# Kernel optimization log

Hardware: AMD Instinct MI355X
Metric: run time of the kernel (lower is better)

## Reference

```python
import jax, jax.numpy as jnp
import numpy as np

TOP_K = 2


def setup_inputs() -> dict:
    key = jax.random.key(0)
    ks = jax.random.split(key, 5)
    T, H, I, E = 4096, 2048, 4096, 8
    scale = 0.02
    return {
        "hidden_states": jax.random.normal(ks[0], (T, H), dtype=jnp.float32),
        "router_logits": jax.random.normal(ks[1], (T, E), dtype=jnp.float32),
        "w1": jax.random.normal(ks[2], (E, I, H), dtype=jnp.float32) * scale,
        "w3": jax.random.normal(ks[3], (E, I, H), dtype=jnp.float32) * scale,
        "w2": jax.random.normal(ks[4], (E, H, I), dtype=jnp.float32) * scale,
    }


def reference(hidden_states, router_logits, w1, w3, w2):
    # hidden_states: [T, H], router_logits: [T, E]
    E = w1.shape[0]
    # Top-k routing with softmax renormalization over the selected logits.
    topk_vals, topk_idx = jax.lax.top_k(router_logits, TOP_K)  # [T, K]
    routing_weights = jax.nn.softmax(topk_vals, axis=-1)       # [T, K]
    # combine[t, e] = sum of routing weights of slots that picked expert e
    combine = jnp.sum(
        jnp.where(topk_idx[:, :, None] == jnp.arange(E)[None, None, :],
                  routing_weights[:, :, None], 0.0),
        axis=1)  # [T, E]
    out = jnp.zeros_like(hidden_states)
    for e in range(E):  # fixed small structural loop over experts
        gate = hidden_states @ w1[e].T        # [T, I]
        up = hidden_states @ w3[e].T          # [T, I]
        y = (jax.nn.silu(gate) * up) @ w2[e].T  # [T, H]
        out = out + combine[:, e, None] * y
    return out
```

## Files before the change

### kernel.cpp

```cpp
#include <hip/hip_runtime.h>
#include <stdint.h>

#define T_TOK 4096
#define H_DIM 2048
#define I_DIM 4096
#define N_EXP 8

typedef __attribute__((ext_vector_type(8))) short bf16x8;
typedef __attribute__((ext_vector_type(4))) float f32x4;
typedef __attribute__((ext_vector_type(8))) unsigned short u16x8;

__device__ __forceinline__ unsigned short f2bf(float x) {
    union { float f; unsigned u; } v; v.f = x;
    unsigned r = v.u + 0x7FFF + ((v.u >> 16) & 1);
    return (unsigned short)(r >> 16);
}

__device__ __forceinline__ void async_cp16(const void* g, const unsigned short* lds_base) {
    __builtin_amdgcn_global_load_lds(
        (const __attribute__((address_space(1))) unsigned*)g,
        (__attribute__((address_space(3))) unsigned*)(unsigned)(uintptr_t)lds_base,
        16, 0, 0);
}

__global__ void routing_kernel(const float* __restrict__ logits,
                               int* __restrict__ counts, int* __restrict__ offsets,
                               int* __restrict__ btok, float* __restrict__ bw,
                               int* __restrict__ tok2slot) {
    __shared__ int s_cnt[N_EXP];
    __shared__ int s_off[N_EXP];
    __shared__ int s_cur[N_EXP];
    const int tid = threadIdx.x;
    if (tid < N_EXP) s_cnt[tid] = 0;
    __syncthreads();

    int e0a[16], e1a[16]; float w0a[16], w1a[16];
    #pragma unroll
    for (int it = 0; it < 16; ++it) {
        int t = tid + it * 256;
        float l[8];
        #pragma unroll
        for (int e = 0; e < 8; ++e) l[e] = logits[t * 8 + e];
        int b0 = 0; float v0 = l[0];
        #pragma unroll
        for (int e = 1; e < 8; ++e) if (l[e] > v0) { v0 = l[e]; b0 = e; }
        int b1 = (b0 == 0) ? 1 : 0; float v1 = l[b1];
        #pragma unroll
        for (int e = 0; e < 8; ++e) if (e != b0 && l[e] > v1) { v1 = l[e]; b1 = e; }
        float w0 = 1.0f / (1.0f + __expf(v1 - v0));
        e0a[it] = b0; e1a[it] = b1; w0a[it] = w0; w1a[it] = 1.0f - w0;
        atomicAdd(&s_cnt[b0], 1);
        atomicAdd(&s_cnt[b1], 1);
    }
    __syncthreads();
    if (tid == 0) {
        int acc = 0;
        for (int e = 0; e < N_EXP; ++e) { s_off[e] = acc; s_cur[e] = acc; acc += s_cnt[e]; }
    }
    __syncthreads();
    if (tid < N_EXP) { counts[tid] = s_cnt[tid]; offsets[tid] = s_off[tid]; }
    #pragma unroll
    for (int it = 0; it < 16; ++it) {
        int t = tid + it * 256;
        int p0 = atomicAdd(&s_cur[e0a[it]], 1);
        btok[p0] = t; bw[p0] = w0a[it];
        int p1 = atomicAdd(&s_cur[e1a[it]], 1);
        btok[p1] = t; bw[p1] = w1a[it];
        tok2slot[2 * t] = p0;
        tok2slot[2 * t + 1] = p1;
    }
}

__global__ void cvt_kernel(const float* __restrict__ x, unsigned short* __restrict__ xb) {
    int i = blockIdx.x * blockDim.x + threadIdx.x;
    float4 v = ((const float4*)x)[i];
    ushort4 o;
    o.x = f2bf(v.x); o.y = f2bf(v.y); o.z = f2bf(v.z); o.w = f2bf(v.w);
    ((ushort4*)xb)[i] = o;
}


__global__ __launch_bounds__(512, 2)
void gemm1p_kernel(const unsigned short* __restrict__ Xb,
                   const unsigned short* __restrict__ W1b,
                   const unsigned short* __restrict__ W3b,
                   const int* __restrict__ counts,
                   const int* __restrict__ offsets,
                   const int* __restrict__ btok,
                   unsigned short* __restrict__ hbuf) {
    const int e = blockIdx.z;
    const int ne = counts[e];
    const int mt = blockIdx.y;
    if (mt * 256 >= ne) return;
    const int nt = blockIdx.x;
    const int off = offsets[e];

    __shared__ unsigned short sA[4][256 * 32];
    __shared__ unsigned short sB1[4][128 * 32];
    __shared__ unsigned short sB3[4][128 * 32];

    const int tid = threadIdx.x;
    const int lane = tid & 63;
    const int wv = tid >> 6;
    const int wm = (wv >> 1) << 6;
    const int wn = (wv & 1) << 6;
    const int q = lane >> 4;
    const int c = lane & 15;
    const int xq = q ^ ((c >> 1) & 3);

    const int aoff = (wm + c) * 32 + xq * 8;
    const int boff = (wn + c) * 32 + xq * 8;

    const int srow = wv * 16 + (lane >> 2);
    const int sg = (lane & 3) ^ ((lane >> 3) & 3);

    int sl0 = mt * 256 + srow;        if (sl0 >= ne) sl0 = ne - 1;
    int sl1 = mt * 256 + srow + 128;  if (sl1 >= ne) sl1 = ne - 1;
    const int tok0 = btok[off + sl0];
    const int tok1 = btok[off + sl1];

    const unsigned short* gA0 = Xb + (size_t)tok0 * H_DIM + sg * 8;
    const unsigned short* gA1 = Xb + (size_t)tok1 * H_DIM + sg * 8;
    const size_t wrow = (size_t)e * I_DIM + nt * 128 + srow;
    const unsigned short* gB1 = W1b + wrow * H_DIM + sg * 8;
    const unsigned short* gB3 = W3b + wrow * H_DIM + sg * 8;

    const int dofsA0 = wv * 512;
    const int dofsA1 = 4096 + wv * 512;
    const int dofsB  = wv * 512;

    f32x4 accg[4][4], accu[4][4];
    const f32x4 zero = {0.0f, 0.0f, 0.0f, 0.0f};
    #pragma unroll
    for (int i = 0; i < 4; ++i)
        #pragma unroll
        for (int j = 0; j < 4; ++j) { accg[i][j] = zero; accu[i][j] = zero; }

    #pragma unroll
    for (int h = 0; h < 3; ++h) {
        const int k = h * 32;
        async_cp16(gA0 + k, &sA[h][dofsA0]);
        async_cp16(gA1 + k, &sA[h][dofsA1]);
        async_cp16(gB1 + k, &sB1[h][dofsB]);
        async_cp16(gB3 + k, &sB3[h][dofsB]);
    }
    asm volatile("s_waitcnt vmcnt(8)" ::: "memory");
    __builtin_amdgcn_s_barrier();
    __builtin_amdgcn_sched_barrier(0);

    const int NT = H_DIM / 32;
    #pragma unroll 4
    for (int h = 0; h < NT; ++h) {
        const unsigned short* pA  = sA[h & 3];
        const unsigned short* pB1 = sB1[h & 3];
        const unsigned short* pB3 = sB3[h & 3];

        bf16x8 af[4], b1f[4], b3f[4];
        #pragma unroll
        for (int i = 0; i < 4; ++i) af[i]  = *(const bf16x8*)(pA  + aoff + i * 512);
        #pragma unroll
        for (int j = 0; j < 4; ++j) b1f[j] = *(const bf16x8*)(pB1 + boff + j * 512);
        #pragma unroll
        for (int j = 0; j < 4; ++j) b3f[j] = *(const bf16x8*)(pB3 + boff + j * 512);

        if (h + 3 < NT) {
            const int r3 = (h + 3) & 3;
            const int k3 = (h + 3) * 32;
            async_cp16(gA0 + k3, &sA[r3][dofsA0]);
            async_cp16(gA1 + k3, &sA[r3][dofsA1]);
            async_cp16(gB1 + k3, &sB1[r3][dofsB]);
            async_cp16(gB3 + k3, &sB3[r3][dofsB]);
        }

        __builtin_amdgcn_s_setprio(1);
        #pragma unroll
        for (int i = 0; i < 4; ++i)
            #pragma unroll
            for (int j = 0; j < 4; ++j)
                accg[i][j] = __builtin_amdgcn_mfma_f32_16x16x32_bf16(af[i], b1f[j], accg[i][j], 0, 0, 0);
        #pragma unroll
        for (int i = 0; i < 4; ++i)
            #pragma unroll
            for (int j = 0; j < 4; ++j)
                accu[i][j] = __builtin_amdgcn_mfma_f32_16x16x32_bf16(af[i], b3f[j], accu[i][j], 0, 0, 0);
        __builtin_amdgcn_s_setprio(0);

        if (h + 1 < NT) {
            if (h + 3 < NT)      asm volatile("s_waitcnt vmcnt(8)" ::: "memory");
            else if (h + 2 < NT) asm volatile("s_waitcnt vmcnt(4)" ::: "memory");
            else                 asm volatile("s_waitcnt vmcnt(0)" ::: "memory");
            __builtin_amdgcn_s_barrier();
            __builtin_amdgcn_sched_barrier(0);
        }
    }

    #pragma unroll
    for (int i = 0; i < 4; ++i) {
        #pragma unroll
        for (int r = 0; r < 4; ++r) {
            int mloc = wm + i * 16 + q * 4 + r;
            int slot = mt * 256 + mloc;
            if (slot < ne) {
                size_t rowbase = (size_t)(off + slot) * I_DIM + nt * 128 + wn;
                #pragma unroll
                for (int j = 0; j < 4; ++j) {
                    float g = accg[i][j][r];
                    float u = accu[i][j][r];
                    float val = (g / (1.0f + __expf(-g))) * u;
                    hbuf[rowbase + j * 16 + c] = f2bf(val);
                }
            }
        }
    }
}

__global__ __launch_bounds__(512, 2)
void gemm2p_kernel(const unsigned short* __restrict__ hbuf,
                   const unsigned short* __restrict__ W2b,
                   const int* __restrict__ counts,
                   const int* __restrict__ offsets,
                   float* __restrict__ ybuf) {
    const int e = blockIdx.z;
    const int ne = counts[e];
    const int mt = blockIdx.y;
    if (mt * 256 >= ne) return;
    const int nt = blockIdx.x;
    const int off = offsets[e];

    __shared__ unsigned short sA[4][256 * 32];
    __shared__ unsigned short sB[4][128 * 32];

    const int tid = threadIdx.x;
    const int lane = tid & 63;
    const int wv = tid >> 6;
    const int wm = (wv >> 1) << 6;
    const int wn = (wv & 1) << 6;
    const int q = lane >> 4;
    const int c = lane & 15;
    const int xq = q ^ ((c >> 1) & 3);

    const int aoff = (wm + c) * 32 + xq * 8;
    const int boff = (wn + c) * 32 + xq * 8;

    const int srow = wv * 16 + (lane >> 2);
    const int sg = (lane & 3) ^ ((lane >> 3) & 3);

    int slot0 = mt * 256 + srow;        if (slot0 >= ne) slot0 = ne - 1;
    int slot1 = mt * 256 + srow + 128;  if (slot1 >= ne) slot1 = ne - 1;
    const unsigned short* gA0 = hbuf + (size_t)(off + slot0) * I_DIM + sg * 8;
    const unsigned short* gA1 = hbuf + (size_t)(off + slot1) * I_DIM + sg * 8;
    const size_t wrow = (size_t)e * H_DIM + nt * 128 + srow;
    const unsigned short* gB = W2b + wrow * I_DIM + sg * 8;

    const int dofsA0 = wv * 512;
    const int dofsA1 = 4096 + wv * 512;
    const int dofsB  = wv * 512;

    f32x4 acc[4][4];
    const f32x4 zero = {0.0f, 0.0f, 0.0f, 0.0f};
    #pragma unroll
    for (int i = 0; i < 4; ++i)
        #pragma unroll
        for (int j = 0; j < 4; ++j) acc[i][j] = zero;

    #pragma unroll
    for (int h = 0; h < 3; ++h) {
        const int k = h * 32;
        async_cp16(gA0 + k, &sA[h][dofsA0]);
        async_cp16(gA1 + k, &sA[h][dofsA1]);
        async_cp16(gB + k,  &sB[h][dofsB]);
    }
    asm volatile("s_waitcnt vmcnt(6)" ::: "memory");
    __builtin_amdgcn_s_barrier();
    __builtin_amdgcn_sched_barrier(0);

    const int NT = I_DIM / 32;
    #pragma unroll 4
    for (int h = 0; h < NT; ++h) {
        const unsigned short* pA = sA[h & 3];
        const unsigned short* pB = sB[h & 3];

        bf16x8 af[4], bfr[4];
        #pragma unroll
        for (int i = 0; i < 4; ++i) af[i]  = *(const bf16x8*)(pA + aoff + i * 512);
        #pragma unroll
        for (int j = 0; j < 4; ++j) bfr[j] = *(const bf16x8*)(pB + boff + j * 512);

        if (h + 3 < NT) {
            const int r3 = (h + 3) & 3;
            const int k3 = (h + 3) * 32;
            async_cp16(gA0 + k3, &sA[r3][dofsA0]);
            async_cp16(gA1 + k3, &sA[r3][dofsA1]);
            async_cp16(gB + k3,  &sB[r3][dofsB]);
        }

        __builtin_amdgcn_s_setprio(1);
        #pragma unroll
        for (int i = 0; i < 4; ++i)
            #pragma unroll
            for (int j = 0; j < 4; ++j)
                acc[i][j] = __builtin_amdgcn_mfma_f32_16x16x32_bf16(af[i], bfr[j], acc[i][j], 0, 0, 0);
        __builtin_amdgcn_s_setprio(0);

        if (h + 1 < NT) {
            if (h + 3 < NT)      asm volatile("s_waitcnt vmcnt(6)" ::: "memory");
            else if (h + 2 < NT) asm volatile("s_waitcnt vmcnt(3)" ::: "memory");
            else                 asm volatile("s_waitcnt vmcnt(0)" ::: "memory");
            __builtin_amdgcn_s_barrier();
            __builtin_amdgcn_sched_barrier(0);
        }
    }

    #pragma unroll
    for (int i = 0; i < 4; ++i) {
        #pragma unroll
        for (int r = 0; r < 4; ++r) {
            int mloc = wm + i * 16 + q * 4 + r;
            int slot = mt * 256 + mloc;
            if (slot < ne) {
                float* obase = ybuf + (size_t)(off + slot) * H_DIM + nt * 128 + wn;
                #pragma unroll
                for (int j = 0; j < 4; ++j)
                    obase[j * 16 + c] = acc[i][j][r];
            }
        }
    }
}

__global__ void combine_kernel(const float* __restrict__ ybuf,
                               const float* __restrict__ bw,
                               const int* __restrict__ tok2slot,
                               float* __restrict__ out) {
    int i = blockIdx.x * blockDim.x + threadIdx.x;
    int t = i >> 9;
    int h4 = i & 511;
    int p0 = tok2slot[2 * t], p1 = tok2slot[2 * t + 1];
    float w0 = bw[p0], w1 = bw[p1];
    float4 a = ((const float4*)(ybuf + (size_t)p0 * H_DIM))[h4];
    float4 b = ((const float4*)(ybuf + (size_t)p1 * H_DIM))[h4];
    float4 o;
    o.x = w0 * a.x + w1 * b.x;
    o.y = w0 * a.y + w1 * b.y;
    o.z = w0 * a.z + w1 * b.z;
    o.w = w0 * a.w + w1 * b.w;
    ((float4*)(out + (size_t)t * H_DIM))[h4] = o;
}


__global__ __launch_bounds__(256, 2)
void gemm1_kernel(const unsigned short* __restrict__ Xb,
                  const float* __restrict__ W1,
                  const float* __restrict__ W3,
                  const int* __restrict__ counts,
                  const int* __restrict__ offsets,
                  const int* __restrict__ btok,
                  unsigned short* __restrict__ hbuf) {
    const int e = blockIdx.z;
    const int ne = counts[e];
    const int mt = blockIdx.y;
    if (mt * 128 >= ne) return;
    const int nt = blockIdx.x;
    const int off = offsets[e];

    __shared__ unsigned short sA[128][32];
    __shared__ unsigned short sB1[128][32];
    __shared__ unsigned short sB3[128][32];
    __shared__ int s_tok[128];

    const int tid = threadIdx.x;
    if (tid < 128) {
        int slot = mt * 128 + tid;
        s_tok[tid] = (slot < ne) ? btok[off + slot] : -1;
    }

    const float* __restrict__ pB1 = W1 + (size_t)e * I_DIM * H_DIM + (size_t)(nt * 128) * H_DIM;
    const float* __restrict__ pB3 = W3 + (size_t)e * I_DIM * H_DIM + (size_t)(nt * 128) * H_DIM;

    const int lane = tid & 63;
    const int wv = tid >> 6;
    const int wm = (wv >> 1) << 6;
    const int wn = (wv & 1) << 6;
    const int q = lane >> 4;
    const int c = lane & 15;

    f32x4 accg[4][4], accu[4][4];
    const f32x4 zero = {0.0f, 0.0f, 0.0f, 0.0f};
    #pragma unroll
    for (int i = 0; i < 4; ++i)
        #pragma unroll
        for (int j = 0; j < 4; ++j) { accg[i][j] = zero; accu[i][j] = zero; }

    const int srow = tid >> 2;
    const int schunk = (tid & 3) * 8;

    for (int kt = 0; kt < H_DIM; kt += 32) {
        __syncthreads();
        #pragma unroll
        for (int p = 0; p < 2; ++p) {
            int r = srow + p * 64;
            int tok = s_tok[r];
            u16x8 av = {0, 0, 0, 0, 0, 0, 0, 0};
            if (tok >= 0)
                av = *(const u16x8*)(Xb + (size_t)tok * H_DIM + kt + schunk);
            *(u16x8*)(&sA[r][schunk]) = av;

            const float* b1 = pB1 + (size_t)r * H_DIM + kt + schunk;
            float4 x0 = *(const float4*)(b1);
            float4 x1 = *(const float4*)(b1 + 4);
            u16x8 bv;
            bv[0] = f2bf(x0.x); bv[1] = f2bf(x0.y); bv[2] = f2bf(x0.z); bv[3] = f2bf(x0.w);
            bv[4] = f2bf(x1.x); bv[5] = f2bf(x1.y); bv[6] = f2bf(x1.z); bv[7] = f2bf(x1.w);
            *(u16x8*)(&sB1[r][schunk]) = bv;

            const float* b3 = pB3 + (size_t)r * H_DIM + kt + schunk;
            float4 y0 = *(const float4*)(b3);
            float4 y1 = *(const float4*)(b3 + 4);
            u16x8 cv;
            cv[0] = f2bf(y0.x); cv[1] = f2bf(y0.y); cv[2] = f2bf(y0.z); cv[3] = f2bf(y0.w);
            cv[4] = f2bf(y1.x); cv[5] = f2bf(y1.y); cv[6] = f2bf(y1.z); cv[7] = f2bf(y1.w);
            *(u16x8*)(&sB3[r][schunk]) = cv;
        }
        __syncthreads();

        bf16x8 af[4], b1f[4], b3f[4];
        #pragma unroll
        for (int i = 0; i < 4; ++i)
            af[i] = *(const bf16x8*)(&sA[wm + i * 16 + c][q * 8]);
        #pragma unroll
        for (int j = 0; j < 4; ++j) {
            b1f[j] = *(const bf16x8*)(&sB1[wn + j * 16 + c][q * 8]);
            b3f[j] = *(const bf16x8*)(&sB3[wn + j * 16 + c][q * 8]);
        }
        #pragma unroll
        for (int i = 0; i < 4; ++i)
            #pragma unroll
            for (int j = 0; j < 4; ++j) {
                accg[i][j] = __builtin_amdgcn_mfma_f32_16x16x32_bf16(af[i], b1f[j], accg[i][j], 0, 0, 0);
                accu[i][j] = __builtin_amdgcn_mfma_f32_16x16x32_bf16(af[i], b3f[j], accu[i][j], 0, 0, 0);
            }
    }

    #pragma unroll
    for (int i = 0; i < 4; ++i) {
        #pragma unroll
        for (int r = 0; r < 4; ++r) {
            int mloc = wm + i * 16 + q * 4 + r;
            int slot = mt * 128 + mloc;
            if (slot < ne) {
                size_t rowbase = (size_t)(off + slot) * I_DIM + nt * 128 + wn;
                #pragma unroll
                for (int j = 0; j < 4; ++j) {
                    float g = accg[i][j][r];
                    float u = accu[i][j][r];
                    float val = (g / (1.0f + __expf(-g))) * u;
                    hbuf[rowbase + j * 16 + c] = f2bf(val);
                }
            }
        }
    }
}

__global__ __launch_bounds__(256, 2)
void gemm2_kernel(const unsigned short* __restrict__ hbuf,
                  const float* __restrict__ W2,
                  const int* __restrict__ counts,
                  const int* __restrict__ offsets,
                  const int* __restrict__ btok,
                  const float* __restrict__ bw,
                  float* __restrict__ out) {
    const int e = blockIdx.z;
    const int ne = counts[e];
    const int mt = blockIdx.y;
    if (mt * 128 >= ne) return;
    const int nt = blockIdx.x;
    const int off = offsets[e];

    __shared__ unsigned short sA[128][32];
    __shared__ unsigned short sB[128][32];

    const int tid = threadIdx.x;
    const int lane = tid & 63;
    const int wv = tid >> 6;
    const int wm = (wv >> 1) << 6;
    const int wn = (wv & 1) << 6;
    const int q = lane >> 4;
    const int c = lane & 15;

    const float* __restrict__ pB = W2 + (size_t)e * H_DIM * I_DIM + (size_t)(nt * 128) * I_DIM;

    f32x4 acc[4][4];
    const f32x4 zero = {0.0f, 0.0f, 0.0f, 0.0f};
    #pragma unroll
    for (int i = 0; i < 4; ++i)
        #pragma unroll
        for (int j = 0; j < 4; ++j) acc[i][j] = zero;

    const int srow = tid >> 2;
    const int schunk = (tid & 3) * 8;

    for (int kt = 0; kt < I_DIM; kt += 32) {
        __syncthreads();
        #pragma unroll
        for (int p = 0; p < 2; ++p) {
            int r = srow + p * 64;
            int slot = mt * 128 + r;
            u16x8 av = {0, 0, 0, 0, 0, 0, 0, 0};
            if (slot < ne)
                av = *(const u16x8*)(hbuf + (size_t)(off + slot) * I_DIM + kt + schunk);
            *(u16x8*)(&sA[r][schunk]) = av;

            const float* b = pB + (size_t)r * I_DIM + kt + schunk;
            float4 x0 = *(const float4*)(b);
            float4 x1 = *(const float4*)(b + 4);
            u16x8 bv;
            bv[0] = f2bf(x0.x); bv[1] = f2bf(x0.y); bv[2] = f2bf(x0.z); bv[3] = f2bf(x0.w);
            bv[4] = f2bf(x1.x); bv[5] = f2bf(x1.y); bv[6] = f2bf(x1.z); bv[7] = f2bf(x1.w);
            *(u16x8*)(&sB[r][schunk]) = bv;
        }
        __syncthreads();

        bf16x8 af[4], bfr[4];
        #pragma unroll
        for (int i = 0; i < 4; ++i)
            af[i] = *(const bf16x8*)(&sA[wm + i * 16 + c][q * 8]);
        #pragma unroll
        for (int j = 0; j < 4; ++j)
            bfr[j] = *(const bf16x8*)(&sB[wn + j * 16 + c][q * 8]);
        #pragma unroll
        for (int i = 0; i < 4; ++i)
            #pragma unroll
            for (int j = 0; j < 4; ++j)
                acc[i][j] = __builtin_amdgcn_mfma_f32_16x16x32_bf16(af[i], bfr[j], acc[i][j], 0, 0, 0);
    }

    #pragma unroll
    for (int i = 0; i < 4; ++i) {
        #pragma unroll
        for (int r = 0; r < 4; ++r) {
            int mloc = wm + i * 16 + q * 4 + r;
            int slot = mt * 128 + mloc;
            if (slot < ne) {
                int tok = btok[off + slot];
                float wgt = bw[off + slot];
                float* obase = out + (size_t)tok * H_DIM + nt * 128 + wn;
                #pragma unroll
                for (int j = 0; j < 4; ++j)
                    atomicAdd(obase + j * 16 + c, wgt * acc[i][j][r]);
            }
        }
    }
}


extern "C" void kernel_launch(void* const* d_in, const int* in_sizes, int n_in,
                              void* d_out, int out_size, void* d_ws, size_t ws_size,
                              hipStream_t stream) {
    const float* hs = (const float*)d_in[0];
    const float* rl = (const float*)d_in[1];
    const float* w1 = (const float*)d_in[2];
    const float* w3 = (const float*)d_in[3];
    const float* w2 = (const float*)d_in[4];
    float* out = (float*)d_out;

    char* ws = (char*)d_ws;
    int*   counts   = (int*)(ws);
    int*   offsets  = (int*)(ws + 256);
    int*   btok     = (int*)(ws + 4096);
    float* bw       = (float*)(ws + 36864);
    int*   tok2slot = (int*)(ws + 69632);

    const size_t MB = 1ull << 20;
    const size_t NEED_A = 529 * MB;

    if (ws_size >= NEED_A) {
        unsigned short* Xb   = (unsigned short*)(ws + 1 * MB);
        unsigned short* hbuf = (unsigned short*)(ws + 17 * MB);
        float*          ybuf = (float*)(ws + 81 * MB);
        unsigned short* w1b  = (unsigned short*)(ws + 145 * MB);
        unsigned short* w3b  = (unsigned short*)(ws + 273 * MB);
        unsigned short* w2b  = (unsigned short*)(ws + 401 * MB);

        routing_kernel<<<1, 256, 0, stream>>>(rl, counts, offsets, btok, bw, tok2slot);

        cvt_kernel<<<(T_TOK * H_DIM / 4) / 256, 256, 0, stream>>>(hs, Xb);
        int wn4 = N_EXP * I_DIM * H_DIM / 4;
        cvt_kernel<<<wn4 / 256, 256, 0, stream>>>(w1, w1b);
        cvt_kernel<<<wn4 / 256, 256, 0, stream>>>(w3, w3b);
        cvt_kernel<<<wn4 / 256, 256, 0, stream>>>(w2, w2b);

        gemm1p_kernel<<<dim3(I_DIM / 128, 32, N_EXP), 512, 0, stream>>>(
            Xb, w1b, w3b, counts, offsets, btok, hbuf);

        gemm2p_kernel<<<dim3(H_DIM / 128, 32, N_EXP), 512, 0, stream>>>(
            hbuf, w2b, counts, offsets, ybuf);

        combine_kernel<<<(T_TOK * (H_DIM / 4)) / 256, 256, 0, stream>>>(
            ybuf, bw, tok2slot, out);
    } else {
        unsigned short* Xb   = (unsigned short*)(ws + 1 * MB);
        unsigned short* hbuf = (unsigned short*)(ws + 32 * MB);

        hipMemsetAsync(out, 0, (size_t)T_TOK * H_DIM * sizeof(float), stream);

        routing_kernel<<<1, 256, 0, stream>>>(rl, counts, offsets, btok, bw, tok2slot);

        cvt_kernel<<<(T_TOK * H_DIM / 4) / 256, 256, 0, stream>>>(hs, Xb);

        gemm1_kernel<<<dim3(I_DIM / 128, T_TOK / 128, N_EXP), 256, 0, stream>>>(
            Xb, w1, w3, counts, offsets, btok, hbuf);

        gemm2_kernel<<<dim3(H_DIM / 128, T_TOK / 128, N_EXP), 256, 0, stream>>>(
            hbuf, w2, counts, offsets, btok, bw, out);
    }
}
```

Baseline: 1.249 ms.

## Double-buffer LDS fragment loads in MoE GEMMs and widen bf16 conversion stores

Both grouped GEMM main loops now read the next k-step's A and B fragments from LDS into a second register set while the current step's MFMAs run. The loop alternates between the two register sets in pairs, and the vmcnt waits are tightened so the next LDS slot is ready one step earlier. This is meant to hide LDS read latency behind matrix math. The fp32-to-bf16 conversion kernel now handles 8 elements per thread with 16-byte stores and half the blocks. The cost is higher register pressure at two waves per SIMD, and the hand-tuned waitcnt values are easy to get wrong.

```diff
diff --git a/kernel.cpp b/kernel.cpp
--- a/kernel.cpp
+++ b/kernel.cpp
@@ -73,10 +73,12 @@
 
 __global__ void cvt_kernel(const float* __restrict__ x, unsigned short* __restrict__ xb) {
     int i = blockIdx.x * blockDim.x + threadIdx.x;
-    float4 v = ((const float4*)x)[i];
-    ushort4 o;
-    o.x = f2bf(v.x); o.y = f2bf(v.y); o.z = f2bf(v.z); o.w = f2bf(v.w);
-    ((ushort4*)xb)[i] = o;
+    float4 a = ((const float4*)x)[2 * i];
+    float4 b = ((const float4*)x)[2 * i + 1];
+    u16x8 o;
+    o[0] = f2bf(a.x); o[1] = f2bf(a.y); o[2] = f2bf(a.z); o[3] = f2bf(a.w);
+    o[4] = f2bf(b.x); o[5] = f2bf(b.y); o[6] = f2bf(b.z); o[7] = f2bf(b.w);
+    ((u16x8*)xb)[i] = o;
 }
 
 
@@ -144,55 +146,69 @@
         async_cp16(gB1 + k, &sB1[h][dofsB]);
         async_cp16(gB3 + k, &sB3[h][dofsB]);
     }
-    asm volatile("s_waitcnt vmcnt(8)" ::: "memory");
+    asm volatile("s_waitcnt vmcnt(4)" ::: "memory");
     __builtin_amdgcn_s_barrier();
     __builtin_amdgcn_sched_barrier(0);
 
     const int NT = H_DIM / 32;
-    #pragma unroll 4
-    for (int h = 0; h < NT; ++h) {
-        const unsigned short* pA  = sA[h & 3];
-        const unsigned short* pB1 = sB1[h & 3];
-        const unsigned short* pB3 = sB3[h & 3];
-
-        bf16x8 af[4], b1f[4], b3f[4];
-        #pragma unroll
-        for (int i = 0; i < 4; ++i) af[i]  = *(const bf16x8*)(pA  + aoff + i * 512);
-        #pragma unroll
-        for (int j = 0; j < 4; ++j) b1f[j] = *(const bf16x8*)(pB1 + boff + j * 512);
-        #pragma unroll
-        for (int j = 0; j < 4; ++j) b3f[j] = *(const bf16x8*)(pB3 + boff + j * 512);
-
-        if (h + 3 < NT) {
-            const int r3 = (h + 3) & 3;
-            const int k3 = (h + 3) * 32;
-            async_cp16(gA0 + k3, &sA[r3][dofsA0]);
-            async_cp16(gA1 + k3, &sA[r3][dofsA1]);
-            async_cp16(gB1 + k3, &sB1[r3][dofsB]);
-            async_cp16(gB3 + k3, &sB3[r3][dofsB]);
-        }
-
-        __builtin_amdgcn_s_setprio(1);
-        #pragma unroll
-        for (int i = 0; i < 4; ++i)
-            #pragma unroll
-            for (int j = 0; j < 4; ++j)
-                accg[i][j] = __builtin_amdgcn_mfma_f32_16x16x32_bf16(af[i], b1f[j], accg[i][j], 0, 0, 0);
-        #pragma unroll
-        for (int i = 0; i < 4; ++i)
-            #pragma unroll
-            for (int j = 0; j < 4; ++j)
-                accu[i][j] = __builtin_amdgcn_mfma_f32_16x16x32_bf16(af[i], b3f[j], accu[i][j], 0, 0, 0);
-        __builtin_amdgcn_s_setprio(0);
-
-        if (h + 1 < NT) {
-            if (h + 3 < NT)      asm volatile("s_waitcnt vmcnt(8)" ::: "memory");
-            else if (h + 2 < NT) asm volatile("s_waitcnt vmcnt(4)" ::: "memory");
-            else                 asm volatile("s_waitcnt vmcnt(0)" ::: "memory");
-            __builtin_amdgcn_s_barrier();
-            __builtin_amdgcn_sched_barrier(0);
-        }
-    }
+    bf16x8 afC[4], b1C[4], afN[4], b1N[4], b3[4];
+    #pragma unroll
+    for (int i = 0; i < 4; ++i) afC[i] = *(const bf16x8*)(&sA[0][aoff + i * 512]);
+    #pragma unroll
+    for (int j = 0; j < 4; ++j) b1C[j] = *(const bf16x8*)(&sB1[0][boff + j * 512]);
+
+#define G1_PHASE(H, AFC, B1C, AFN, B1N)                                                              \
+    {                                                                                                \
+        const int slotC = (H) & 3;                                                                   \
+        _Pragma("unroll")                                                                            \
+        for (int j = 0; j < 4; ++j)                                                                  \
+            b3[j] = *(const bf16x8*)(&sB3[slotC][boff + j * 512]);                                   \
+        if ((H) + 1 < NT) {                                                                          \
+            const int slotN = ((H) + 1) & 3;                                                         \
+            _Pragma("unroll")                                                                        \
+            for (int i = 0; i < 4; ++i)                                                              \
+                AFN[i] = *(const bf16x8*)(&sA[slotN][aoff + i * 512]);                               \
+            _Pragma("unroll")                                                                        \
+            for (int j = 0; j < 4; ++j)                                                              \
+                B1N[j] = *(const bf16x8*)(&sB1[slotN][boff + j * 512]);                              \
+        }                                                                                            \
+        if ((H) + 3 < NT) {                                                                          \
+            const int r3 = ((H) + 3) & 3;                                                            \
+            const int k3 = ((H) + 3) * 32;                                                           \
+            async_cp16(gA0 + k3, &sA[r3][dofsA0]);                                                   \
+            async_cp16(gA1 + k3, &sA[r3][dofsA1]);                                                   \
+            async_cp16(gB1 + k3, &sB1[r3][dofsB]);                                                   \
+            async_cp16(gB3 + k3, &sB3[r3][dofsB]);                                                   \
+        }                                                                                            \
+        __builtin_amdgcn_sched_barrier(0);                                                           \
+        __builtin_amdgcn_s_setprio(1);                                                               \
+        _Pragma("unroll")                                                                            \
+        for (int i = 0; i < 4; ++i)                                                                  \
+            _Pragma("unroll")                                                                        \
+            for (int j = 0; j < 4; ++j)                                                              \
+                accg[i][j] = __builtin_amdgcn_mfma_f32_16x16x32_bf16(AFC[i], B1C[j], accg[i][j], 0, 0, 0); \
+        _Pragma("unroll")                                                                            \
+        for (int i = 0; i < 4; ++i)                                                                  \
+            _Pragma("unroll")                                                                        \
+            for (int j = 0; j < 4; ++j)                                                              \
+                accu[i][j] = __builtin_amdgcn_mfma_f32_16x16x32_bf16(AFC[i], b3[j], accu[i][j], 0, 0, 0);  \
+        __builtin_amdgcn_s_setprio(0);                                                               \
+        if ((H) + 1 < NT) {                                                                          \
+            asm volatile("s_waitcnt lgkmcnt(8)" ::: "memory");                                       \
+            if ((H) + 2 < NT) {                                                                      \
+                if ((H) + 3 < NT) asm volatile("s_waitcnt vmcnt(4)" ::: "memory");                   \
+                else              asm volatile("s_waitcnt vmcnt(0)" ::: "memory");                   \
+            }                                                                                        \
+            __builtin_amdgcn_s_barrier();                                                            \
+            __builtin_amdgcn_sched_barrier(0);                                                       \
+        }                                                                                            \
+    }
+
+    for (int h = 0; h < NT; h += 2) {
+        G1_PHASE(h,     afC, b1C, afN, b1N);
+        G1_PHASE(h + 1, afN, b1N, afC, b1C);
+    }
+#undef G1_PHASE
 
     #pragma unroll
     for (int i = 0; i < 4; ++i) {
@@ -270,46 +286,59 @@
         async_cp16(gA1 + k, &sA[h][dofsA1]);
         async_cp16(gB + k,  &sB[h][dofsB]);
     }
-    asm volatile("s_waitcnt vmcnt(6)" ::: "memory");
+    asm volatile("s_waitcnt vmcnt(3)" ::: "memory");
     __builtin_amdgcn_s_barrier();
     __builtin_amdgcn_sched_barrier(0);
 
     const int NT = I_DIM / 32;
-    #pragma unroll 4
-    for (int h = 0; h < NT; ++h) {
-        const unsigned short* pA = sA[h & 3];
-        const unsigned short* pB = sB[h & 3];
-
-        bf16x8 af[4], bfr[4];
-        #pragma unroll
-        for (int i = 0; i < 4; ++i) af[i]  = *(const bf16x8*)(pA + aoff + i * 512);
-        #pragma unroll
-        for (int j = 0; j < 4; ++j) bfr[j] = *(const bf16x8*)(pB + boff + j * 512);
-
-        if (h + 3 < NT) {
-            const int r3 = (h + 3) & 3;
-            const int k3 = (h + 3) * 32;
-            async_cp16(gA0 + k3, &sA[r3][dofsA0]);
-            async_cp16(gA1 + k3, &sA[r3][dofsA1]);
-            async_cp16(gB + k3,  &sB[r3][dofsB]);
-        }
-
-        __builtin_amdgcn_s_setprio(1);
-        #pragma unroll
-        for (int i = 0; i < 4; ++i)
-            #pragma unroll
-            for (int j = 0; j < 4; ++j)
-                acc[i][j] = __builtin_amdgcn_mfma_f32_16x16x32_bf16(af[i], bfr[j], acc[i][j], 0, 0, 0);
-        __builtin_amdgcn_s_setprio(0);
-
-        if (h + 1 < NT) {
-            if (h + 3 < NT)      asm volatile("s_waitcnt vmcnt(6)" ::: "memory");
-            else if (h + 2 < NT) asm volatile("s_waitcnt vmcnt(3)" ::: "memory");
-            else                 asm volatile("s_waitcnt vmcnt(0)" ::: "memory");
-            __builtin_amdgcn_s_barrier();
-            __builtin_amdgcn_sched_barrier(0);
-        }
-    }
+    bf16x8 afC[4], bC[4], afN[4], bN[4];
+    #pragma unroll
+    for (int i = 0; i < 4; ++i) afC[i] = *(const bf16x8*)(&sA[0][aoff + i * 512]);
+    #pragma unroll
+    for (int j = 0; j < 4; ++j) bC[j]  = *(const bf16x8*)(&sB[0][boff + j * 512]);
+
+#define G2_PHASE(H, AFC, BC, AFN, BN)                                                                \
+    {                                                                                                \
+        if ((H) + 1 < NT) {                                                                          \
+            const int slotN = ((H) + 1) & 3;                                                         \
+            _Pragma("unroll")                                                                        \
+            for (int i = 0; i < 4; ++i)                                                              \
+                AFN[i] = *(const bf16x8*)(&sA[slotN][aoff + i * 512]);                               \
+            _Pragma("unroll")                                                                        \
+            for (int j = 0; j < 4; ++j)                                                              \
+                BN[j] = *(const bf16x8*)(&sB[slotN][boff + j * 512]);                                \
+        }                                                                                            \
+        if ((H) + 3 < NT) {                                                                          \
+            const int r3 = ((H) + 3) & 3;                                                            \
+            const int k3 = ((H) + 3) * 32;                                                           \
+            async_cp16(gA0 + k3, &sA[r3][dofsA0]);                                                   \
+            async_cp16(gA1 + k3, &sA[r3][dofsA1]);                                                   \
+            async_cp16(gB + k3,  &sB[r3][dofsB]);                                                    \
+        }                                                                                            \
+        __builtin_amdgcn_sched_barrier(0);                                                           \
+        __builtin_amdgcn_s_setprio(1);                                                               \
+        _Pragma("unroll")                                                                            \
+        for (int i = 0; i < 4; ++i)                                                                  \
+            _Pragma("unroll")                                                                        \
+            for (int j = 0; j < 4; ++j)                                                              \
+                acc[i][j] = __builtin_amdgcn_mfma_f32_16x16x32_bf16(AFC[i], BC[j], acc[i][j], 0, 0, 0); \
+        __builtin_amdgcn_s_setprio(0);                                                               \
+        if ((H) + 1 < NT) {                                                                          \
+            asm volatile("s_waitcnt lgkmcnt(8)" ::: "memory");                                       \
+            if ((H) + 2 < NT) {                                                                      \
+                if ((H) + 3 < NT) asm volatile("s_waitcnt vmcnt(3)" ::: "memory");                   \
+                else              asm volatile("s_waitcnt vmcnt(0)" ::: "memory");                   \
+            }                                                                                        \
+            __builtin_amdgcn_s_barrier();                                                            \
+            __builtin_amdgcn_sched_barrier(0);                                                       \
+        }                                                                                            \
+    }
+
+    for (int h = 0; h < NT; h += 2) {
+        G2_PHASE(h,     afC, bC, afN, bN);
+        G2_PHASE(h + 1, afN, bN, afC, bC);
+    }
+#undef G2_PHASE
 
     #pragma unroll
     for (int i = 0; i < 4; ++i) {
@@ -582,11 +611,11 @@
 
         routing_kernel<<<1, 256, 0, stream>>>(rl, counts, offsets, btok, bw, tok2slot);
 
-        cvt_kernel<<<(T_TOK * H_DIM / 4) / 256, 256, 0, stream>>>(hs, Xb);
-        int wn4 = N_EXP * I_DIM * H_DIM / 4;
-        cvt_kernel<<<wn4 / 256, 256, 0, stream>>>(w1, w1b);
-        cvt_kernel<<<wn4 / 256, 256, 0, stream>>>(w3, w3b);
-        cvt_kernel<<<wn4 / 256, 256, 0, stream>>>(w2, w2b);
+        cvt_kernel<<<(T_TOK * H_DIM / 8) / 256, 256, 0, stream>>>(hs, Xb);
+        int wn8 = N_EXP * I_DIM * H_DIM / 8;
+        cvt_kernel<<<wn8 / 256, 256, 0, stream>>>(w1, w1b);
+        cvt_kernel<<<wn8 / 256, 256, 0, stream>>>(w3, w3b);
+        cvt_kernel<<<wn8 / 256, 256, 0, stream>>>(w2, w2b);
 
         gemm1p_kernel<<<dim3(I_DIM / 128, 32, N_EXP), 512, 0, stream>>>(
             Xb, w1b, w3b, counts, offsets, btok, hbuf);
@@ -604,7 +633,7 @@
 
         routing_kernel<<<1, 256, 0, stream>>>(rl, counts, offsets, btok, bw, tok2slot);
 
-        cvt_kernel<<<(T_TOK * H_DIM / 4) / 256, 256, 0, stream>>>(hs, Xb);
+        cvt_kernel<<<(T_TOK * H_DIM / 8) / 256, 256, 0, stream>>>(hs, Xb);
 
         gemm1_kernel<<<dim3(I_DIM / 128, T_TOK / 128, N_EXP), 256, 0, stream>>>(
             Xb, w1, w3, counts, offsets, btok, hbuf);
```

New measurement: 1.272 ms. No clear change (+1.8%).

## Fuse fp32-to-bf16 weight conversion into grouped GEMM loads and widen gemm2 tile

Applied to the files above, without the earlier changes.

Drops the three separate weight conversion kernels and their bf16 staging buffers. The GEMM kernels now read fp32 weights directly, convert them in registers and write them to LDS, using a 2-stage lookahead in place of async copies. gemm2 moves to a 256x256 tile with 8x4 accumulators per wave, which halves its N grid. The cvt kernel now processes 8 elements per thread. The cost is twice the weight bytes read inside the GEMMs, plus conversion ALU work and higher register pressure in the main loops.

```diff
diff --git a/kernel.cpp b/kernel.cpp
--- a/kernel.cpp
+++ b/kernel.cpp
@@ -14,6 +14,13 @@
     union { float f; unsigned u; } v; v.f = x;
     unsigned r = v.u + 0x7FFF + ((v.u >> 16) & 1);
     return (unsigned short)(r >> 16);
+}
+
+__device__ __forceinline__ u16x8 cvt8(float4 a, float4 b) {
+    u16x8 o;
+    o[0] = f2bf(a.x); o[1] = f2bf(a.y); o[2] = f2bf(a.z); o[3] = f2bf(a.w);
+    o[4] = f2bf(b.x); o[5] = f2bf(b.y); o[6] = f2bf(b.z); o[7] = f2bf(b.w);
+    return o;
 }
 
 __device__ __forceinline__ void async_cp16(const void* g, const unsigned short* lds_base) {
@@ -73,17 +80,16 @@
 
 __global__ void cvt_kernel(const float* __restrict__ x, unsigned short* __restrict__ xb) {
     int i = blockIdx.x * blockDim.x + threadIdx.x;
-    float4 v = ((const float4*)x)[i];
-    ushort4 o;
-    o.x = f2bf(v.x); o.y = f2bf(v.y); o.z = f2bf(v.z); o.w = f2bf(v.w);
-    ((ushort4*)xb)[i] = o;
+    float4 a = ((const float4*)x)[2 * i];
+    float4 b = ((const float4*)x)[2 * i + 1];
+    ((u16x8*)xb)[i] = cvt8(a, b);
 }
 
 
 __global__ __launch_bounds__(512, 2)
 void gemm1p_kernel(const unsigned short* __restrict__ Xb,
-                   const unsigned short* __restrict__ W1b,
-                   const unsigned short* __restrict__ W3b,
+                   const float* __restrict__ W1,
+                   const float* __restrict__ W3,
                    const int* __restrict__ counts,
                    const int* __restrict__ offsets,
                    const int* __restrict__ btok,
@@ -122,12 +128,12 @@
     const unsigned short* gA0 = Xb + (size_t)tok0 * H_DIM + sg * 8;
     const unsigned short* gA1 = Xb + (size_t)tok1 * H_DIM + sg * 8;
     const size_t wrow = (size_t)e * I_DIM + nt * 128 + srow;
-    const unsigned short* gB1 = W1b + wrow * H_DIM + sg * 8;
-    const unsigned short* gB3 = W3b + wrow * H_DIM + sg * 8;
+    const float* gW1 = W1 + wrow * H_DIM + (lane & 3) * 8;
+    const float* gW3 = W3 + wrow * H_DIM + (lane & 3) * 8;
+    const int bwro = srow * 32 + sg * 8;
 
     const int dofsA0 = wv * 512;
     const int dofsA1 = 4096 + wv * 512;
-    const int dofsB  = wv * 512;
 
     f32x4 accg[4][4], accu[4][4];
     const f32x4 zero = {0.0f, 0.0f, 0.0f, 0.0f};
@@ -136,42 +142,55 @@
         #pragma unroll
         for (int j = 0; j < 4; ++j) { accg[i][j] = zero; accu[i][j] = zero; }
 
-    #pragma unroll
-    for (int h = 0; h < 3; ++h) {
-        const int k = h * 32;
-        async_cp16(gA0 + k, &sA[h][dofsA0]);
-        async_cp16(gA1 + k, &sA[h][dofsA1]);
-        async_cp16(gB1 + k, &sB1[h][dofsB]);
-        async_cp16(gB3 + k, &sB3[h][dofsB]);
-    }
-    asm volatile("s_waitcnt vmcnt(8)" ::: "memory");
+    {
+        float4 a0 = *(const float4*)(gW1);
+        float4 a1 = *(const float4*)(gW1 + 4);
+        float4 b0 = *(const float4*)(gW3);
+        float4 b1 = *(const float4*)(gW3 + 4);
+        float4 c0 = *(const float4*)(gW1 + 32);
+        float4 c1 = *(const float4*)(gW1 + 36);
+        float4 d0 = *(const float4*)(gW3 + 32);
+        float4 d1 = *(const float4*)(gW3 + 36);
+        *(u16x8*)(&sB1[0][bwro]) = cvt8(a0, a1);
+        *(u16x8*)(&sB3[0][bwro]) = cvt8(b0, b1);
+        *(u16x8*)(&sB1[1][bwro]) = cvt8(c0, c1);
+        *(u16x8*)(&sB3[1][bwro]) = cvt8(d0, d1);
+    }
+    async_cp16(gA0,      &sA[0][dofsA0]);
+    async_cp16(gA1,      &sA[0][dofsA1]);
+    async_cp16(gA0 + 32, &sA[1][dofsA0]);
+    async_cp16(gA1 + 32, &sA[1][dofsA1]);
+    asm volatile("s_waitcnt lgkmcnt(0)" ::: "memory");
+    asm volatile("s_waitcnt vmcnt(2)" ::: "memory");
     __builtin_amdgcn_s_barrier();
     __builtin_amdgcn_sched_barrier(0);
 
     const int NT = H_DIM / 32;
     #pragma unroll 4
     for (int h = 0; h < NT; ++h) {
-        const unsigned short* pA  = sA[h & 3];
-        const unsigned short* pB1 = sB1[h & 3];
-        const unsigned short* pB3 = sB3[h & 3];
-
+        const int cs = h & 3;
         bf16x8 af[4], b1f[4], b3f[4];
         #pragma unroll
-        for (int i = 0; i < 4; ++i) af[i]  = *(const bf16x8*)(pA  + aoff + i * 512);
-        #pragma unroll
-        for (int j = 0; j < 4; ++j) b1f[j] = *(const bf16x8*)(pB1 + boff + j * 512);
-        #pragma unroll
-        for (int j = 0; j < 4; ++j) b3f[j] = *(const bf16x8*)(pB3 + boff + j * 512);
-
-        if (h + 3 < NT) {
-            const int r3 = (h + 3) & 3;
-            const int k3 = (h + 3) * 32;
-            async_cp16(gA0 + k3, &sA[r3][dofsA0]);
-            async_cp16(gA1 + k3, &sA[r3][dofsA1]);
-            async_cp16(gB1 + k3, &sB1[r3][dofsB]);
-            async_cp16(gB3 + k3, &sB3[r3][dofsB]);
-        }
-
+        for (int i = 0; i < 4; ++i) af[i]  = *(const bf16x8*)(&sA[cs][aoff + i * 512]);
+        #pragma unroll
+        for (int j = 0; j < 4; ++j) b1f[j] = *(const bf16x8*)(&sB1[cs][boff + j * 512]);
+        #pragma unroll
+        for (int j = 0; j < 4; ++j) b3f[j] = *(const bf16x8*)(&sB3[cs][boff + j * 512]);
+
+        const bool stg = (h + 2) < NT;
+        float4 r10, r11, r30, r31;
+        if (stg) {
+            const float* p1 = gW1 + (size_t)(h + 2) * 32;
+            const float* p3 = gW3 + (size_t)(h + 2) * 32;
+            r10 = *(const float4*)(p1);
+            r11 = *(const float4*)(p1 + 4);
+            r30 = *(const float4*)(p3);
+            r31 = *(const float4*)(p3 + 4);
+            const int ns = (h + 2) & 3;
+            async_cp16(gA0 + (h + 2) * 32, &sA[ns][dofsA0]);
+            async_cp16(gA1 + (h + 2) * 32, &sA[ns][dofsA1]);
+        }
+        __builtin_amdgcn_sched_barrier(0);
         __builtin_amdgcn_s_setprio(1);
         #pragma unroll
         for (int i = 0; i < 4; ++i)
@@ -185,10 +204,15 @@
                 accu[i][j] = __builtin_amdgcn_mfma_f32_16x16x32_bf16(af[i], b3f[j], accu[i][j], 0, 0, 0);
         __builtin_amdgcn_s_setprio(0);
 
+        if (stg) {
+            const int ns = (h + 2) & 3;
+            *(u16x8*)(&sB1[ns][bwro]) = cvt8(r10, r11);
+            *(u16x8*)(&sB3[ns][bwro]) = cvt8(r30, r31);
+        }
         if (h + 1 < NT) {
-            if (h + 3 < NT)      asm volatile("s_waitcnt vmcnt(8)" ::: "memory");
-            else if (h + 2 < NT) asm volatile("s_waitcnt vmcnt(4)" ::: "memory");
-            else                 asm volatile("s_waitcnt vmcnt(0)" ::: "memory");
+            asm volatile("s_waitcnt lgkmcnt(0)" ::: "memory");
+            if (stg) asm volatile("s_waitcnt vmcnt(2)" ::: "memory");
+            else     asm volatile("s_waitcnt vmcnt(0)" ::: "memory");
             __builtin_amdgcn_s_barrier();
             __builtin_amdgcn_sched_barrier(0);
         }
@@ -216,7 +240,7 @@
 
 __global__ __launch_bounds__(512, 2)
 void gemm2p_kernel(const unsigned short* __restrict__ hbuf,
-                   const unsigned short* __restrict__ W2b,
+                   const float* __restrict__ W2,
                    const int* __restrict__ counts,
                    const int* __restrict__ offsets,
                    float* __restrict__ ybuf) {
@@ -228,13 +252,13 @@
     const int off = offsets[e];
 
     __shared__ unsigned short sA[4][256 * 32];
-    __shared__ unsigned short sB[4][128 * 32];
+    __shared__ unsigned short sB[4][256 * 32];
 
     const int tid = threadIdx.x;
     const int lane = tid & 63;
     const int wv = tid >> 6;
-    const int wm = (wv >> 1) << 6;
-    const int wn = (wv & 1) << 6;
+    const int wm = (wv >> 2) << 7;
+    const int wn = (wv & 3) << 6;
     const int q = lane >> 4;
     const int c = lane & 15;
     const int xq = q ^ ((c >> 1) & 3);
@@ -249,76 +273,98 @@
     int slot1 = mt * 256 + srow + 128;  if (slot1 >= ne) slot1 = ne - 1;
     const unsigned short* gA0 = hbuf + (size_t)(off + slot0) * I_DIM + sg * 8;
     const unsigned short* gA1 = hbuf + (size_t)(off + slot1) * I_DIM + sg * 8;
-    const size_t wrow = (size_t)e * H_DIM + nt * 128 + srow;
-    const unsigned short* gB = W2b + wrow * I_DIM + sg * 8;
+    const size_t wrow = (size_t)e * H_DIM + nt * 256 + srow;
+    const float* gB0 = W2 + wrow * I_DIM + (lane & 3) * 8;
+    const float* gB1 = gB0 + (size_t)128 * I_DIM;
+    const int bwro = srow * 32 + sg * 8;
 
     const int dofsA0 = wv * 512;
     const int dofsA1 = 4096 + wv * 512;
-    const int dofsB  = wv * 512;
-
-    f32x4 acc[4][4];
+
+    f32x4 acc[8][4];
     const f32x4 zero = {0.0f, 0.0f, 0.0f, 0.0f};
     #pragma unroll
-    for (int i = 0; i < 4; ++i)
+    for (int i = 0; i < 8; ++i)
         #pragma unroll
         for (int j = 0; j < 4; ++j) acc[i][j] = zero;
 
-    #pragma unroll
-    for (int h = 0; h < 3; ++h) {
-        const int k = h * 32;
-        async_cp16(gA0 + k, &sA[h][dofsA0]);
-        async_cp16(gA1 + k, &sA[h][dofsA1]);
-        async_cp16(gB + k,  &sB[h][dofsB]);
-    }
-    asm volatile("s_waitcnt vmcnt(6)" ::: "memory");
+    {
+        float4 a0 = *(const float4*)(gB0);
+        float4 a1 = *(const float4*)(gB0 + 4);
+        float4 b0 = *(const float4*)(gB1);
+        float4 b1 = *(const float4*)(gB1 + 4);
+        float4 c0 = *(const float4*)(gB0 + 32);
+        float4 c1 = *(const float4*)(gB0 + 36);
+        float4 d0 = *(const float4*)(gB1 + 32);
+        float4 d1 = *(const float4*)(gB1 + 36);
+        *(u16x8*)(&sB[0][bwro])        = cvt8(a0, a1);
+        *(u16x8*)(&sB[0][bwro + 4096]) = cvt8(b0, b1);
+        *(u16x8*)(&sB[1][bwro])        = cvt8(c0, c1);
+        *(u16x8*)(&sB[1][bwro + 4096]) = cvt8(d0, d1);
+    }
+    async_cp16(gA0,      &sA[0][dofsA0]);
+    async_cp16(gA1,      &sA[0][dofsA1]);
+    async_cp16(gA0 + 32, &sA[1][dofsA0]);
+    async_cp16(gA1 + 32, &sA[1][dofsA1]);
+    asm volatile("s_waitcnt lgkmcnt(0)" ::: "memory");
+    asm volatile("s_waitcnt vmcnt(2)" ::: "memory");
     __builtin_amdgcn_s_barrier();
     __builtin_amdgcn_sched_barrier(0);
 
     const int NT = I_DIM / 32;
     #pragma unroll 4
     for (int h = 0; h < NT; ++h) {
-        const unsigned short* pA = sA[h & 3];
-        const unsigned short* pB = sB[h & 3];
-
-        bf16x8 af[4], bfr[4];
-        #pragma unroll
-        for (int i = 0; i < 4; ++i) af[i]  = *(const bf16x8*)(pA + aoff + i * 512);
-        #pragma unroll
-        for (int j = 0; j < 4; ++j) bfr[j] = *(const bf16x8*)(pB + boff + j * 512);
-
-        if (h + 3 < NT) {
-            const int r3 = (h + 3) & 3;
-            const int k3 = (h + 3) * 32;
-            async_cp16(gA0 + k3, &sA[r3][dofsA0]);
-            async_cp16(gA1 + k3, &sA[r3][dofsA1]);
-            async_cp16(gB + k3,  &sB[r3][dofsB]);
-        }
-
+        const int cs = h & 3;
+        bf16x8 af[8], bfr[4];
+        #pragma unroll
+        for (int i = 0; i < 8; ++i) af[i]  = *(const bf16x8*)(&sA[cs][aoff + i * 512]);
+        #pragma unroll
+        for (int j = 0; j < 4; ++j) bfr[j] = *(const bf16x8*)(&sB[cs][boff + j * 512]);
+
+        const bool stg = (h + 2) < NT;
+        float4 r00, r01, r10, r11;
+        if (stg) {
+            const float* p0 = gB0 + (size_t)(h + 2) * 32;
+            const float* p1 = gB1 + (size_t)(h + 2) * 32;
+            r00 = *(const float4*)(p0);
+            r01 = *(const float4*)(p0 + 4);
+            r10 = *(const float4*)(p1);
+            r11 = *(const float4*)(p1 + 4);
+            const int ns = (h + 2) & 3;
+            async_cp16(gA0 + (h + 2) * 32, &sA[ns][dofsA0]);
+            async_cp16(gA1 + (h + 2) * 32, &sA[ns][dofsA1]);
+        }
+        __builtin_amdgcn_sched_barrier(0);
         __builtin_amdgcn_s_setprio(1);
         #pragma unroll
-        for (int i = 0; i < 4; ++i)
+        for (int i = 0; i < 8; ++i)
             #pragma unroll
             for (int j = 0; j < 4; ++j)
                 acc[i][j] = __builtin_amdgcn_mfma_f32_16x16x32_bf16(af[i], bfr[j], acc[i][j], 0, 0, 0);
         __builtin_amdgcn_s_setprio(0);
 
+        if (stg) {
+            const int ns = (h + 2) & 3;
+            *(u16x8*)(&sB[ns][bwro])        = cvt8(r00, r01);
+            *(u16x8*)(&sB[ns][bwro + 4096]) = cvt8(r10, r11);
+        }
         if (h + 1 < NT) {
-            if (h + 3 < NT)      asm volatile("s_waitcnt vmcnt(6)" ::: "memory");
-            else if (h + 2 < NT) asm volatile("s_waitcnt vmcnt(3)" ::: "memory");
-            else                 asm volatile("s_waitcnt vmcnt(0)" ::: "memory");
+            asm volatile("s_waitcnt lgkmcnt(0)" ::: "memory");
+            if (stg) asm volatile("s_waitcnt vmcnt(2)" ::: "memory");
+            else     asm volatile("s_waitcnt vmcnt(0)" ::: "memory");
             __builtin_amdgcn_s_barrier();
             __builtin_amdgcn_sched_barrier(0);
         }
     }
 
     #pragma unroll
-    for (int i = 0; i < 4; ++i) {
+    for (int i = 0; i < 8; ++i) {
         #pragma unroll
         for (int r = 0; r < 4; ++r) {
             int mloc = wm + i * 16 + q * 4 + r;
             int slot = mt * 256 + mloc;
             if (slot < ne) {
-                float* obase = ybuf + (size_t)(off + slot) * H_DIM + nt * 128 + wn;
+                float* obase = ybuf + (size_t)(off + slot) * H_DIM + nt * 256 + wn;
                 #pragma unroll
                 for (int j = 0; j < 4; ++j)
                     obase[j * 16 + c] = acc[i][j][r];
@@ -405,20 +451,10 @@
             *(u16x8*)(&sA[r][schunk]) = av;
 
             const float* b1 = pB1 + (size_t)r * H_DIM + kt + schunk;
-            float4 x0 = *(const float4*)(b1);
-            float4 x1 = *(const float4*)(b1 + 4);
-            u16x8 bv;
-            bv[0] = f2bf(x0.x); bv[1] = f2bf(x0.y); bv[2] = f2bf(x0.z); bv[3] = f2bf(x0.w);
-            bv[4] = f2bf(x1.x); bv[5] = f2bf(x1.y); bv[6] = f2bf(x1.z); bv[7] = f2bf(x1.w);
-            *(u16x8*)(&sB1[r][schunk]) = bv;
+            *(u16x8*)(&sB1[r][schunk]) = cvt8(*(const float4*)(b1), *(const float4*)(b1 + 4));
 
             const float* b3 = pB3 + (size_t)r * H_DIM + kt + schunk;
-            float4 y0 = *(const float4*)(b3);
-            float4 y1 = *(const float4*)(b3 + 4);
-            u16x8 cv;
-            cv[0] = f2bf(y0.x); cv[1] = f2bf(y0.y); cv[2] = f2bf(y0.z); cv[3] = f2bf(y0.w);
-            cv[4] = f2bf(y1.x); cv[5] = f2bf(y1.y); cv[6] = f2bf(y1.z); cv[7] = f2bf(y1.w);
-            *(u16x8*)(&sB3[r][schunk]) = cv;
+            *(u16x8*)(&sB3[r][schunk]) = cvt8(*(const float4*)(b3), *(const float4*)(b3 + 4));
         }
         __syncthreads();
 
@@ -510,12 +546,7 @@
             *(u16x8*)(&sA[r][schunk]) = av;
 
             const float* b = pB + (size_t)r * I_DIM + kt + schunk;
-            float4 x0 = *(const float4*)(b);
-            float4 x1 = *(const float4*)(b + 4);
-            u16x8 bv;
-            bv[0] = f2bf(x0.x); bv[1] = f2bf(x0.y); bv[2] = f2bf(x0.z); bv[3] = f2bf(x0.w);
-            bv[4] = f2bf(x1.x); bv[5] = f2bf(x1.y); bv[6] = f2bf(x1.z); bv[7] = f2bf(x1.w);
-            *(u16x8*)(&sB[r][schunk]) = bv;
+            *(u16x8*)(&sB[r][schunk]) = cvt8(*(const float4*)(b), *(const float4*)(b + 4));
         }
         __syncthreads();
 
@@ -570,29 +601,22 @@
     int*   tok2slot = (int*)(ws + 69632);
 
     const size_t MB = 1ull << 20;
-    const size_t NEED_A = 529 * MB;
+    const size_t NEED_A = 146 * MB;
 
     if (ws_size >= NEED_A) {
         unsigned short* Xb   = (unsigned short*)(ws + 1 * MB);
         unsigned short* hbuf = (unsigned short*)(ws + 17 * MB);
         float*          ybuf = (float*)(ws + 81 * MB);
-        unsigned short* w1b  = (unsigned short*)(ws + 145 * MB);
-        unsigned short* w3b  = (unsigned short*)(ws + 273 * MB);
-        unsigned short* w2b  = (unsigned short*)(ws + 401 * MB);
 
         routing_kernel<<<1, 256, 0, stream>>>(rl, counts, offsets, btok, bw, tok2slot);
 
-        cvt_kernel<<<(T_TOK * H_DIM / 4) / 256, 256, 0, stream>>>(hs, Xb);
-        int wn4 = N_EXP * I_DIM * H_DIM / 4;
-        cvt_kernel<<<wn4 / 256, 256, 0, stream>>>(w1, w1b);
-        cvt_kernel<<<wn4 / 256, 256, 0, stream>>>(w3, w3b);
-        cvt_kernel<<<wn4 / 256, 256, 0, stream>>>(w2, w2b);
+        cvt_kernel<<<(T_TOK * H_DIM / 8) / 256, 256, 0, stream>>>(hs, Xb);
 
         gemm1p_kernel<<<dim3(I_DIM / 128, 32, N_EXP), 512, 0, stream>>>(
-            Xb, w1b, w3b, counts, offsets, btok, hbuf);
-
-        gemm2p_kernel<<<dim3(H_DIM / 128, 32, N_EXP), 512, 0, stream>>>(
-            hbuf, w2b, counts, offsets, ybuf);
+            Xb, w1, w3, counts, offsets, btok, hbuf);
+
+        gemm2p_kernel<<<dim3(H_DIM / 256, 32, N_EXP), 512, 0, stream>>>(
+            hbuf, w2, counts, offsets, ybuf);
 
         combine_kernel<<<(T_TOK * (H_DIM / 4)) / 256, 256, 0, stream>>>(
             ybuf, bw, tok2slot, out);
@@ -604,7 +628,7 @@
 
         routing_kernel<<<1, 256, 0, stream>>>(rl, counts, offsets, btok, bw, tok2slot);
 
-        cvt_kernel<<<(T_TOK * H_DIM / 4) / 256, 256, 0, stream>>>(hs, Xb);
+        cvt_kernel<<<(T_TOK * H_DIM / 8) / 256, 256, 0, stream>>>(hs, Xb);
 
         gemm1_kernel<<<dim3(I_DIM / 128, T_TOK / 128, N_EXP), 256, 0, stream>>>(
             Xb, w1, w3, counts, offsets, btok, hbuf);
```

After: 1.465 ms. +17.3%, slower.
